# Kernel tuning notes

Hardware: AMD Instinct MI355X
Metric: run time of the kernel (lower is better)

Reference implementation:

```python
import jax, jax.numpy as jnp
import numpy as np

N, E, K, F_IN, H = 50000, 640000, 3, 128, 128


def setup_inputs() -> dict:
    key = jax.random.key(0)
    ks = jax.random.split(key, 14)
    s = 0.05
    return {
        "x": jax.random.normal(ks[0], (N, F_IN), jnp.float32),
        "edge_index": jax.random.randint(ks[1], (2, E), 0, N, dtype=jnp.int32),
        "edge_weight": jax.random.uniform(ks[2], (E,), jnp.float32, minval=0.1, maxval=1.0),
        "W_x": jax.random.normal(ks[3], (4, F_IN, H), jnp.float32) * s,   # dense input weights (i,f,c,o)
        "w_c": jax.random.normal(ks[4], (3, H), jnp.float32) * s,         # peephole weights (i,f,o)
        "b": jax.random.normal(ks[5], (4, H), jnp.float32) * s,           # gate biases (i,f,c,o)
        "theta": jax.random.normal(ks[6], (4, K, H, H), jnp.float32) * s, # ChebConv weights per gate
        "theta_b": jax.random.normal(ks[7], (4, H), jnp.float32) * s,     # ChebConv biases per gate
        "gcn_w": jax.random.normal(ks[8], (H, H), jnp.float32) * s,
        "gcn_b": jnp.zeros((H,), jnp.float32),
        "bn_gamma": jnp.ones((H,), jnp.float32),
        "bn_beta": jnp.zeros((H,), jnp.float32),
        "bn_mean": jax.random.normal(ks[9], (H,), jnp.float32) * 0.1,
        "bn_var": jax.random.uniform(ks[10], (H,), jnp.float32, minval=0.5, maxval=1.5),
        "lin_w": jax.random.normal(ks[11], (H, 1), jnp.float32) * s,
        "lin_b": jnp.zeros((1,), jnp.float32),
    }


def reference(x, edge_index, edge_weight, W_x, w_c, b, theta, theta_b, gcn_w, gcn_b, bn_gamma, bn_beta, bn_mean, bn_var, lin_w, lin_b):
    n = x.shape[0]
    src, dst = edge_index[0], edge_index[1]

    # --- ChebConv normalization (sym, lambda_max=2): L_hat = -D^{-1/2} A D^{-1/2}, zero diagonal ---
    deg = jnp.zeros((n,), x.dtype).at[src].add(edge_weight)
    safe = jnp.where(deg > 0, deg, 1.0)
    dis = jnp.where(deg > 0, jax.lax.rsqrt(safe), 0.0)
    lw = -dis[src] * edge_weight * dis[dst]  # per-edge scaled-Laplacian weight

    def prop(h):  # out[i] = sum_{edges j->i} lw * h[j]
        return jnp.zeros_like(h).at[dst].add(lw[:, None] * h[src])

    def cheb(h, th, tb):  # sum_k T_k(L_hat) h @ theta_k + bias, Chebyshev recurrence
        Tx0, out = h, h @ th[0]
        Tx1 = prop(h)
        out = out + Tx1 @ th[1]
        for k in range(2, K):
            Tx2 = 2.0 * prop(Tx1) - Tx0
            out = out + Tx2 @ th[k]
            Tx0, Tx1 = Tx1, Tx2
        return out + tb

    # --- GCLSTM with H = C = 0 (module passes no initial state) ---
    Hs = jnp.zeros((n, W_x.shape[2]), x.dtype)
    Cs = jnp.zeros_like(Hs)
    I = jax.nn.sigmoid(x @ W_x[0] + cheb(Hs, theta[0], theta_b[0]) + w_c[0] * Cs + b[0])
    Fg = jax.nn.sigmoid(x @ W_x[1] + cheb(Hs, theta[1], theta_b[1]) + w_c[1] * Cs + b[1])
    T = jnp.tanh(x @ W_x[2] + cheb(Hs, theta[2], theta_b[2]) + b[2])
    Cs = Fg * Cs + I * T
    O = jax.nn.sigmoid(x @ W_x[3] + cheb(Hs, theta[3], theta_b[3]) + w_c[2] * Cs + b[3])
    Hs = O * jnp.tanh(Cs)

    # --- GCNConv(H) with unit edge weights + added self-loops ---
    h = Hs @ gcn_w
    deg_g = jnp.ones((n,), x.dtype).at[dst].add(jnp.ones((edge_index.shape[1],), x.dtype))
    dg = jax.lax.rsqrt(deg_g)
    g = jnp.zeros_like(h).at[dst].add((dg[src] * dg[dst])[:, None] * h[src]) + (dg * dg)[:, None] * h + gcn_b

    g = jax.nn.relu(g)
    g = bn_gamma * (g - bn_mean) * jax.lax.rsqrt(bn_var + 1e-5) + bn_beta  # BatchNorm1d (eval)
    return g @ lin_w + lin_b  # Dropout = identity in eval
```

## Files before the change

kernel.cpp:

```cpp
#include <hip/hip_runtime.h>
#include <hip/hip_bf16.h>

#define NN 50000
#define NE 640000
#define CAP 64
#define NGB 782
#define NBIN 782
#define NA 196
#define EPA 3328
#define ORow 784

typedef unsigned short ushort_t;
typedef unsigned int uint_t;
typedef __attribute__((ext_vector_type(8))) short bf16x8;
typedef __attribute__((ext_vector_type(4))) float f32x4;

__device__ __forceinline__ float b2f(ushort_t u) {
    union { uint_t u; float f; } v; v.u = ((uint_t)u) << 16; return v.f;
}
__device__ __forceinline__ ushort_t f2b(float f) {
    union { float f; uint_t u; } v; v.f = f;
    uint_t u = v.u;
    uint_t r = u + 0x7fffu + ((u >> 16) & 1u);
    return (ushort_t)(r >> 16);
}
__device__ __forceinline__ float fsig(float x)  { return __builtin_amdgcn_rcpf(1.0f + __expf(-x)); }
__device__ __forceinline__ float ftanh(float x) { return 1.0f - 2.0f * __builtin_amdgcn_rcpf(1.0f + __expf(2.0f * x)); }
__device__ __forceinline__ float ldm(const void* p, int i, int mf) {
    return mf ? ((const float*)p)[i] : b2f(((const ushort_t*)p)[i]);
}

#define OFF_HB    0
#define OFF_BSRC  12800000
#define OFF_CNT   25600000
#define OFF_CHUNK 25800000
#define OFF_OFFS  28409152
#define OFF_WT    29023808
#define OFF_COEF  29154880
#define OFF_MODE  29157444
#define WS_REQ    29157448

__global__ void fb_k(ushort_t* __restrict__ out, int n) {
    int i = blockIdx.x * blockDim.x + threadIdx.x;
    if (i < n) out[i] = 0;
}

__global__ void prep_k(const ushort_t* __restrict__ x,
                       const void* __restrict__ Wx, const void* __restrict__ gcnw,
                       const void* __restrict__ wc, const void* __restrict__ bb,
                       const void* __restrict__ thb,
                       const void* __restrict__ gam, const void* __restrict__ bet,
                       const void* __restrict__ mea, const void* __restrict__ var,
                       const void* __restrict__ linw, const void* __restrict__ linb,
                       ushort_t* __restrict__ WT, float* __restrict__ coef,
                       int* __restrict__ mode) {
    __shared__ int si[256];
    __shared__ float red[128];
    int b = blockIdx.x, t = threadIdx.x;
    int bad = 0;
    for (int i = t; i < 4096; i += 256) {
        int e = (x[i] >> 7) & 0xFF;
        if (e >= 0xC0) bad++;
    }
    si[t] = bad; __syncthreads();
    for (int o = 128; o >= 1; o >>= 1) { if (t < o) si[t] += si[t + o]; __syncthreads(); }
    int mf = (si[0] > 8) ? 1 : 0;

    if (b < 32) {
        int gid = b * 256 + t;
        int m  = gid >> 11;
        int u  = gid & 2047;
        int k  = u >> 4;
        int f0 = (u & 15) << 3;
        const int srcoff[4] = { 0, 2 * 16384, 3 * 16384, 0 };
        const void* S = (m == 3) ? gcnw : Wx;
        int sbase = srcoff[m] + k * 128 + f0;
        ushort_t vals[8];
        if (mf == 0) {
            bf16x8 v = *(const bf16x8*)((const ushort_t*)S + sbase);
            #pragma unroll
            for (int i = 0; i < 8; i++) vals[i] = (ushort_t)v[i];
        } else {
            const float* Sf = (const float*)S + sbase;
            #pragma unroll
            for (int i = 0; i < 8; i++) vals[i] = f2b(Sf[i]);
        }
        ushort_t* D = WT + m * 16384 + k;
        #pragma unroll
        for (int i = 0; i < 8; i++) D[(f0 + i) * 128] = vals[i];
    } else {
        if (t < 128) {
            float rs = rsqrtf(ldm(var, t, mf) + 1e-5f);
            float ga = ldm(gam, t, mf);
            float lw = ldm(linw, t, mf);
            coef[t]       = ldm(thb, t, mf)           + ldm(bb, t, mf);
            coef[128 + t] = ldm(thb, 2 * 128 + t, mf) + ldm(bb, 2 * 128 + t, mf);
            coef[256 + t] = ldm(thb, 3 * 128 + t, mf) + ldm(bb, 3 * 128 + t, mf);
            coef[384 + t] = ldm(wc, 2 * 128 + t, mf);
            coef[512 + t] = ga * rs * lw;
            red[t] = (ldm(bet, t, mf) - ldm(mea, t, mf) * ga * rs) * lw;
        }
        __syncthreads();
        for (int off = 64; off >= 1; off >>= 1) {
            if (t < off && t < 128) red[t] += red[t + off];
            __syncthreads();
        }
        if (t == 0) {
            coef[640] = red[0] + ldm(linb, 0, mf);
            mode[0] = mf;
        }
    }
}

__launch_bounds__(256)
__global__ void gafi_k(const void* __restrict__ x, const ushort_t* __restrict__ WT,
                       const float* __restrict__ coef, const int* __restrict__ mode,
                       ushort_t* __restrict__ hb,
                       const int* __restrict__ ei, uint_t* __restrict__ chunk,
                       int* __restrict__ offs) {
    __shared__ int sh[4352];
    ushort_t* tile = (ushort_t*)sh;
    int per = blockIdx.x / 5, rem = blockIdx.x % 5;
    int t = threadIdx.x;

    if (rem == 4) {
        int a = per;
        int e0 = a * EPA; if (e0 > NE) e0 = NE;
        int e1 = e0 + EPA; if (e1 > NE) e1 = NE;
        const int* dstp = ei + NE;
        for (int i = t; i < NBIN; i += 256) sh[i] = 0;
        __syncthreads();
        for (int i = e0 + t; i < e1; i += 256) atomicAdd(&sh[dstp[i] >> 6], 1);
        __syncthreads();
        int b0 = t * 4;
        int s = 0;
        #pragma unroll
        for (int j = 0; j < 4; j++) { int bi = b0 + j; if (bi < NBIN) s += sh[bi]; }
        sh[1024 + t] = s;
        __syncthreads();
        for (int off = 1; off < 256; off <<= 1) {
            int v = (t >= off) ? sh[1024 + t - off] : 0;
            __syncthreads();
            sh[1024 + t] += v;
            __syncthreads();
        }
        int run = (t == 0) ? 0 : sh[1024 + t - 1];
        int* orow = offs + a * ORow;
        #pragma unroll
        for (int j = 0; j < 4; j++) {
            int bi = b0 + j;
            if (bi < NBIN) {
                int c = sh[bi];
                orow[bi] = run;
                sh[bi] = run;
                run += c;
            }
        }
        if (t == 0) orow[NBIN] = e1 - e0;
        __syncthreads();
        uint_t* ck = chunk + a * EPA;
        for (int i = e0 + t; i < e1; i += 256) {
            int d = dstp[i], sn = ei[i];
            int pos = atomicAdd(&sh[d >> 6], 1);
            ck[pos] = ((uint_t)sn << 6) | (uint_t)(d & 63);
        }
        return;
    }

    int gb = per * 4 + rem;
    if (gb >= NGB) return;
    int base = gb * 64;
    int mf = mode[0];

    for (int i = 0; i < 4; i++) {
        int idx = (i * 256 + t) * 8;
        int row = idx >> 7, col = idx & 127;
        int n = base + row;
        bf16x8 v;
        if (n >= NN) {
            v = (bf16x8)0;
        } else if (mf == 0) {
            v = *(const bf16x8*)((const ushort_t*)x + n * 128 + col);
        } else {
            const float* xf = (const float*)x + n * 128 + col;
            float4 lo = *(const float4*)xf;
            float4 hi = *(const float4*)(xf + 4);
            v[0] = (short)f2b(lo.x); v[1] = (short)f2b(lo.y);
            v[2] = (short)f2b(lo.z); v[3] = (short)f2b(lo.w);
            v[4] = (short)f2b(hi.x); v[5] = (short)f2b(hi.y);
            v[6] = (short)f2b(hi.z); v[7] = (short)f2b(hi.w);
        }
        *(bf16x8*)&tile[row * 136 + col] = v;
    }
    __syncthreads();

    int lane = t & 63, wave = t >> 6;
    int m = lane & 15, quad = lane >> 4;

    bf16x8 a[4][4];
    #pragma unroll
    for (int rt = 0; rt < 4; rt++)
        #pragma unroll
        for (int kt = 0; kt < 4; kt++)
            a[rt][kt] = *(const bf16x8*)&tile[(rt * 16 + m) * 136 + kt * 32 + quad * 8];
    __syncthreads();

    const ushort_t* WTi = WT;
    const ushort_t* WTc = WT + 16384;
    const ushort_t* WTo = WT + 2 * 16384;

    #pragma unroll
    for (int ft = 0; ft < 2; ft++) {
        int f = wave * 32 + ft * 16 + m;
        bf16x8 bi[4], bc[4], bo[4];
        #pragma unroll
        for (int kt = 0; kt < 4; kt++) {
            int off = f * 128 + kt * 32 + quad * 8;
            bi[kt] = *(const bf16x8*)(WTi + off);
            bc[kt] = *(const bf16x8*)(WTc + off);
            bo[kt] = *(const bf16x8*)(WTo + off);
        }
        float bi_f = coef[f], bc_f = coef[128 + f], bo_f = coef[256 + f], w2 = coef[384 + f];
        #pragma unroll
        for (int rt = 0; rt < 4; rt++) {
            f32x4 ai = {0,0,0,0}, ac = {0,0,0,0}, ao = {0,0,0,0};
            #pragma unroll
            for (int kt = 0; kt < 4; kt++) {
                ai = __builtin_amdgcn_mfma_f32_16x16x32_bf16(a[rt][kt], bi[kt], ai, 0, 0, 0);
                ac = __builtin_amdgcn_mfma_f32_16x16x32_bf16(a[rt][kt], bc[kt], ac, 0, 0, 0);
                ao = __builtin_amdgcn_mfma_f32_16x16x32_bf16(a[rt][kt], bo[kt], ao, 0, 0, 0);
            }
            #pragma unroll
            for (int r = 0; r < 4; r++) {
                float I  = fsig(ai[r] + bi_f);
                float T  = ftanh(ac[r] + bc_f);
                float Cs = I * T;
                float O  = fsig(ao[r] + w2 * Cs + bo_f);
                float Hs = O * ftanh(Cs);
                tile[(rt * 16 + quad * 4 + r) * 136 + f] = f2b(Hs);
            }
        }
    }
    __syncthreads();

    const ushort_t* WTg = WT + 3 * 16384;
    bf16x8 ah[4][4];
    #pragma unroll
    for (int rt = 0; rt < 4; rt++)
        #pragma unroll
        for (int kt = 0; kt < 4; kt++)
            ah[rt][kt] = *(const bf16x8*)&tile[(rt * 16 + m) * 136 + kt * 32 + quad * 8];

    #pragma unroll
    for (int ft = 0; ft < 2; ft++) {
        int f = wave * 32 + ft * 16 + m;
        bf16x8 bg[4];
        #pragma unroll
        for (int kt = 0; kt < 4; kt++)
            bg[kt] = *(const bf16x8*)(WTg + f * 128 + kt * 32 + quad * 8);
        #pragma unroll
        for (int rt = 0; rt < 4; rt++) {
            f32x4 acc = {0,0,0,0};
            #pragma unroll
            for (int kt = 0; kt < 4; kt++)
                acc = __builtin_amdgcn_mfma_f32_16x16x32_bf16(ah[rt][kt], bg[kt], acc, 0, 0, 0);
            #pragma unroll
            for (int r = 0; r < 4; r++) {
                int n = base + rt * 16 + quad * 4 + r;
                if (n < NN) hb[n * 128 + f] = f2b(acc[r]);
            }
        }
    }
}

__launch_bounds__(256)
__global__ void scat_k(const uint_t* __restrict__ chunk, const int* __restrict__ offs,
                       int* __restrict__ bsrc, int* __restrict__ cnt) {
    __shared__ int sstart[NA];
    __shared__ int P[256];
    __shared__ int lcnt[64];
    __shared__ uint_t lbuck[64 * CAP];
    int b = blockIdx.x, t = threadIdx.x;
    int node0 = b << 6;
    if (t < 64) lcnt[t] = 0;
    int len = 0;
    if (t < NA) {
        int st = offs[t * ORow + b];
        int en = offs[t * ORow + b + 1];
        sstart[t] = st;
        len = en - st;
    }
    P[t] = len;
    __syncthreads();
    for (int off = 1; off < 256; off <<= 1) {
        int v = (t >= off) ? P[t - off] : 0;
        __syncthreads();
        P[t] += v;
        __syncthreads();
    }
    int T = P[255];
    for (int i = t; i < T; i += 256) {
        int lo = 0, hi = NA - 1;
        while (lo < hi) { int mid = (lo + hi) >> 1; if (P[mid] > i) hi = mid; else lo = mid + 1; }
        int prev = (lo == 0) ? 0 : P[lo - 1];
        uint_t w = chunk[lo * EPA + sstart[lo] + (i - prev)];
        int d6 = (int)(w & 63u);
        int sn = (int)(w >> 6);
        int p = atomicAdd(&lcnt[d6], 1);
        if (p < CAP) lbuck[(d6 << 6) + p] = (uint_t)sn;
    }
    __syncthreads();
    if (t < 64) { int node = node0 + t; if (node < NN) cnt[node] = lcnt[t]; }
    const int4* lb4 = (const int4*)lbuck;
    int4* bs4 = (int4*)bsrc;
    for (int i = t; i < 1024; i += 256) {
        int node = node0 + (i >> 4);
        if (node < NN) bs4[(node0 << 4) + i] = lb4[i];
    }
}

__launch_bounds__(256)
__global__ void gat_out_k(const ushort_t* __restrict__ hb, const int* __restrict__ cnt,
                          const int* __restrict__ bsrc,
                          const void* __restrict__ gcnb, const float* __restrict__ coef,
                          const int* __restrict__ mode, void* __restrict__ out) {
    int wid  = (blockIdx.x * blockDim.x + threadIdx.x) >> 6;
    int lane = threadIdx.x & 63;
    if (wid >= NN) return;
    int half = lane >> 5, sl = lane & 31;
    int c = cnt[wid]; if (c < 0) c = 0;
    int deg = (c < CAP) ? c : CAP;
    const int* brow = bsrc + wid * CAP;

    float a0 = 0.0f, a1 = 0.0f, a2 = 0.0f, a3 = 0.0f;
    int s0 = brow[half];
    int s1 = brow[half + 2];
    for (int j = half; j < deg; j += 4) {
        int sn0 = brow[(j + 4) & (CAP - 1)];
        int sn1 = brow[(j + 6) & (CAP - 1)];
        {
            int cs = cnt[s0]; if (cs < 0) cs = 0;
            uint2 r = *(const uint2*)(hb + s0 * 128 + sl * 4);
            float w = rsqrtf(1.0f + (float)cs);
            a0 += w * b2f((ushort_t)(r.x & 0xffffu));
            a1 += w * b2f((ushort_t)(r.x >> 16));
            a2 += w * b2f((ushort_t)(r.y & 0xffffu));
            a3 += w * b2f((ushort_t)(r.y >> 16));
        }
        if (j + 2 < deg) {
            int cs = cnt[s1]; if (cs < 0) cs = 0;
            uint2 r = *(const uint2*)(hb + s1 * 128 + sl * 4);
            float w = rsqrtf(1.0f + (float)cs);
            a0 += w * b2f((ushort_t)(r.x & 0xffffu));
            a1 += w * b2f((ushort_t)(r.x >> 16));
            a2 += w * b2f((ushort_t)(r.y & 0xffffu));
            a3 += w * b2f((ushort_t)(r.y >> 16));
        }
        s0 = sn0; s1 = sn1;
    }
    float d = rsqrtf(1.0f + (float)c);
    if (half == 0) {
        uint2 r = *(const uint2*)(hb + wid * 128 + sl * 4);
        a0 += d * b2f((ushort_t)(r.x & 0xffffu));
        a1 += d * b2f((ushort_t)(r.x >> 16));
        a2 += d * b2f((ushort_t)(r.y & 0xffffu));
        a3 += d * b2f((ushort_t)(r.y >> 16));
    }
    a0 += __shfl_xor(a0, 32); a1 += __shfl_xor(a1, 32);
    a2 += __shfl_xor(a2, 32); a3 += __shfl_xor(a3, 32);
    int mf = mode[0];
    int fb = sl * 4;
    float g0 = d * a0 + ldm(gcnb, fb,     mf);
    float g1 = d * a1 + ldm(gcnb, fb + 1, mf);
    float g2 = d * a2 + ldm(gcnb, fb + 2, mf);
    float g3 = d * a3 + ldm(gcnb, fb + 3, mf);
    float v = fmaxf(g0, 0.0f) * coef[512 + fb]
            + fmaxf(g1, 0.0f) * coef[512 + fb + 1]
            + fmaxf(g2, 0.0f) * coef[512 + fb + 2]
            + fmaxf(g3, 0.0f) * coef[512 + fb + 3];
    #pragma unroll
    for (int o = 32; o >= 1; o >>= 1) v += __shfl_down(v, o);
    if (lane == 0) {
        float r = 0.5f * v + coef[640];
        if (mf) ((float*)out)[wid] = r;
        else    ((ushort_t*)out)[wid] = f2b(r);
    }
}

extern "C" void kernel_launch(void* const* d_in, const int* in_sizes, int n_in,
                              void* d_out, int out_size, void* d_ws, size_t ws_size,
                              hipStream_t stream) {
    if (ws_size < (size_t)WS_REQ) {
        fb_k<<<(out_size + 255) / 256, 256, 0, stream>>>((ushort_t*)d_out, out_size);
        return;
    }
    const void* x    = d_in[0];
    const int*  ei   = (const int*)d_in[1];
    const void* Wx   = d_in[3];
    const void* wc   = d_in[4];
    const void* bb   = d_in[5];
    const void* thb  = d_in[7];
    const void* gcnw = d_in[8];
    const void* gcnb = d_in[9];
    const void* gam  = d_in[10];
    const void* bet  = d_in[11];
    const void* mea  = d_in[12];
    const void* var  = d_in[13];
    const void* linw = d_in[14];
    const void* linb = d_in[15];

    char* ws = (char*)d_ws;
    ushort_t* hb    = (ushort_t*)(ws + OFF_HB);
    int*      bsrc  = (int*)     (ws + OFF_BSRC);
    int*      cnt   = (int*)     (ws + OFF_CNT);
    uint_t*   chunk = (uint_t*)  (ws + OFF_CHUNK);
    int*      offs  = (int*)     (ws + OFF_OFFS);
    ushort_t* WT    = (ushort_t*)(ws + OFF_WT);
    float*    coef  = (float*)   (ws + OFF_COEF);
    int*      mode  = (int*)     (ws + OFF_MODE);

    prep_k<<<33, 256, 0, stream>>>((const ushort_t*)x, Wx, gcnw, wc, bb, thb,
                                   gam, bet, mea, var, linw, linb, WT, coef, mode);
    gafi_k<<<NA * 5, 256, 0, stream>>>(x, WT, coef, mode, hb, ei, chunk, offs);
    scat_k<<<NBIN, 256, 0, stream>>>(chunk, offs, bsrc, cnt);
    gat_out_k<<<(NN * 64 + 255) / 256, 256, 0, stream>>>(hb, cnt, bsrc, gcnb, coef, mode, d_out);
}
```

Before: 177.6 us.

## Restructure pipeline: fuse binning into prep, compute counts with GEMM, gather from LDS buckets

Edge binning now runs in the prep kernel, so the gate GEMM kernel only interleaves GEMM blocks with per-bin degree counting. The old scatter kernel and the gather/output kernel are merged: each bin block builds its source buckets in shared memory and its four waves gather and reduce 16 nodes each. This removes the global bsrc array and one launch. The trade-offs are that degree counting reads the chunk array twice, and the gather now runs on fewer, longer-lived blocks with less parallelism per node.

```diff
diff --git a/kernel.cpp b/kernel.cpp
--- a/kernel.cpp
+++ b/kernel.cpp
@@ -31,43 +31,90 @@
 }
 
 #define OFF_HB    0
-#define OFF_BSRC  12800000
-#define OFF_CNT   25600000
-#define OFF_CHUNK 25800000
-#define OFF_OFFS  28409152
-#define OFF_WT    29023808
-#define OFF_COEF  29154880
-#define OFF_MODE  29157444
-#define WS_REQ    29157448
+#define OFF_CHUNK 12800000
+#define OFF_OFFS  15409152
+#define OFF_CNT   16023808
+#define OFF_WT    16223808
+#define OFF_COEF  16354880
+#define OFF_MODE  16357444
+#define WS_REQ    16357448
 
 __global__ void fb_k(ushort_t* __restrict__ out, int n) {
     int i = blockIdx.x * blockDim.x + threadIdx.x;
     if (i < n) out[i] = 0;
 }
 
-__global__ void prep_k(const ushort_t* __restrict__ x,
-                       const void* __restrict__ Wx, const void* __restrict__ gcnw,
-                       const void* __restrict__ wc, const void* __restrict__ bb,
-                       const void* __restrict__ thb,
-                       const void* __restrict__ gam, const void* __restrict__ bet,
-                       const void* __restrict__ mea, const void* __restrict__ var,
-                       const void* __restrict__ linw, const void* __restrict__ linb,
-                       ushort_t* __restrict__ WT, float* __restrict__ coef,
-                       int* __restrict__ mode) {
-    __shared__ int si[256];
+__launch_bounds__(256)
+__global__ void bsprep_k(const ushort_t* __restrict__ x, const int* __restrict__ ei,
+                         const void* __restrict__ Wx, const void* __restrict__ gcnw,
+                         const void* __restrict__ wc, const void* __restrict__ bb,
+                         const void* __restrict__ thb,
+                         const void* __restrict__ gam, const void* __restrict__ bet,
+                         const void* __restrict__ mea, const void* __restrict__ var,
+                         const void* __restrict__ linw, const void* __restrict__ linb,
+                         ushort_t* __restrict__ WT, float* __restrict__ coef,
+                         int* __restrict__ mode,
+                         uint_t* __restrict__ chunk, int* __restrict__ offs) {
+    __shared__ int sh[1280];
     __shared__ float red[128];
     int b = blockIdx.x, t = threadIdx.x;
+
+    if (b < NA) {
+        int a = b;
+        int e0 = a * EPA; if (e0 > NE) e0 = NE;
+        int e1 = e0 + EPA; if (e1 > NE) e1 = NE;
+        const int* dstp = ei + NE;
+        for (int i = t; i < NBIN; i += 256) sh[i] = 0;
+        __syncthreads();
+        for (int i = e0 + t; i < e1; i += 256) atomicAdd(&sh[dstp[i] >> 6], 1);
+        __syncthreads();
+        int b0 = t * 4;
+        int s = 0;
+        #pragma unroll
+        for (int j = 0; j < 4; j++) { int bi = b0 + j; if (bi < NBIN) s += sh[bi]; }
+        sh[1024 + t] = s;
+        __syncthreads();
+        for (int off = 1; off < 256; off <<= 1) {
+            int v = (t >= off) ? sh[1024 + t - off] : 0;
+            __syncthreads();
+            sh[1024 + t] += v;
+            __syncthreads();
+        }
+        int run = (t == 0) ? 0 : sh[1024 + t - 1];
+        int* orow = offs + a * ORow;
+        #pragma unroll
+        for (int j = 0; j < 4; j++) {
+            int bi = b0 + j;
+            if (bi < NBIN) {
+                int c = sh[bi];
+                orow[bi] = run;
+                sh[bi] = run;
+                run += c;
+            }
+        }
+        if (t == 0) orow[NBIN] = e1 - e0;
+        __syncthreads();
+        uint_t* ck = chunk + a * EPA;
+        for (int i = e0 + t; i < e1; i += 256) {
+            int d = dstp[i], sn = ei[i];
+            int pos = atomicAdd(&sh[d >> 6], 1);
+            ck[pos] = ((uint_t)sn << 6) | (uint_t)(d & 63);
+        }
+        return;
+    }
+
     int bad = 0;
     for (int i = t; i < 4096; i += 256) {
         int e = (x[i] >> 7) & 0xFF;
         if (e >= 0xC0) bad++;
     }
-    si[t] = bad; __syncthreads();
-    for (int o = 128; o >= 1; o >>= 1) { if (t < o) si[t] += si[t + o]; __syncthreads(); }
-    int mf = (si[0] > 8) ? 1 : 0;
-
-    if (b < 32) {
-        int gid = b * 256 + t;
+    sh[t] = bad; __syncthreads();
+    for (int o = 128; o >= 1; o >>= 1) { if (t < o) sh[t] += sh[t + o]; __syncthreads(); }
+    int mf = (sh[0] > 8) ? 1 : 0;
+
+    int wb = b - NA;
+    if (wb < 32) {
+        int gid = wb * 256 + t;
         int m  = gid >> 11;
         int u  = gid & 2047;
         int k  = u >> 4;
@@ -113,62 +160,50 @@
 }
 
 __launch_bounds__(256)
-__global__ void gafi_k(const void* __restrict__ x, const ushort_t* __restrict__ WT,
-                       const float* __restrict__ coef, const int* __restrict__ mode,
-                       ushort_t* __restrict__ hb,
-                       const int* __restrict__ ei, uint_t* __restrict__ chunk,
-                       int* __restrict__ offs) {
-    __shared__ int sh[4352];
-    ushort_t* tile = (ushort_t*)sh;
-    int per = blockIdx.x / 5, rem = blockIdx.x % 5;
-    int t = threadIdx.x;
-
-    if (rem == 4) {
-        int a = per;
-        int e0 = a * EPA; if (e0 > NE) e0 = NE;
-        int e1 = e0 + EPA; if (e1 > NE) e1 = NE;
-        const int* dstp = ei + NE;
-        for (int i = t; i < NBIN; i += 256) sh[i] = 0;
-        __syncthreads();
-        for (int i = e0 + t; i < e1; i += 256) atomicAdd(&sh[dstp[i] >> 6], 1);
-        __syncthreads();
-        int b0 = t * 4;
-        int s = 0;
-        #pragma unroll
-        for (int j = 0; j < 4; j++) { int bi = b0 + j; if (bi < NBIN) s += sh[bi]; }
-        sh[1024 + t] = s;
+__global__ void gacnt_k(const void* __restrict__ x, const ushort_t* __restrict__ WT,
+                        const float* __restrict__ coef, const int* __restrict__ mode,
+                        ushort_t* __restrict__ hb,
+                        const uint_t* __restrict__ chunk, const int* __restrict__ offs,
+                        int* __restrict__ cnt) {
+    __shared__ __align__(16) char smem[17408];
+    int b = blockIdx.x, t = threadIdx.x;
+
+    if (b & 1) {
+        int bin = b >> 1;
+        int* P      = (int*)smem;
+        int* sstart = (int*)(smem + 1024);
+        int* lcnt   = (int*)(smem + 1808);
+        if (t < 64) lcnt[t] = 0;
+        int len = 0;
+        if (t < NA) {
+            int st = offs[t * ORow + bin];
+            int en = offs[t * ORow + bin + 1];
+            sstart[t] = st;
+            len = en - st;
+        }
+        P[t] = len;
         __syncthreads();
         for (int off = 1; off < 256; off <<= 1) {
-            int v = (t >= off) ? sh[1024 + t - off] : 0;
+            int v = (t >= off) ? P[t - off] : 0;
             __syncthreads();
-            sh[1024 + t] += v;
+            P[t] += v;
             __syncthreads();
         }
-        int run = (t == 0) ? 0 : sh[1024 + t - 1];
-        int* orow = offs + a * ORow;
-        #pragma unroll
-        for (int j = 0; j < 4; j++) {
-            int bi = b0 + j;
-            if (bi < NBIN) {
-                int c = sh[bi];
-                orow[bi] = run;
-                sh[bi] = run;
-                run += c;
-            }
-        }
-        if (t == 0) orow[NBIN] = e1 - e0;
-        __syncthreads();
-        uint_t* ck = chunk + a * EPA;
-        for (int i = e0 + t; i < e1; i += 256) {
-            int d = dstp[i], sn = ei[i];
-            int pos = atomicAdd(&sh[d >> 6], 1);
-            ck[pos] = ((uint_t)sn << 6) | (uint_t)(d & 63);
-        }
+        int T = P[255];
+        for (int i = t; i < T; i += 256) {
+            int lo = 0, hi = NA - 1;
+            while (lo < hi) { int mid = (lo + hi) >> 1; if (P[mid] > i) hi = mid; else lo = mid + 1; }
+            int prev = (lo == 0) ? 0 : P[lo - 1];
+            uint_t w = chunk[lo * EPA + sstart[lo] + (i - prev)];
+            atomicAdd(&lcnt[(int)(w & 63u)], 1);
+        }
+        __syncthreads();
+        if (t < 64) { int node = (bin << 6) + t; if (node < NN) cnt[node] = lcnt[t]; }
         return;
     }
 
-    int gb = per * 4 + rem;
-    if (gb >= NGB) return;
+    ushort_t* tile = (ushort_t*)smem;
+    int gb = b >> 1;
     int base = gb * 64;
     int mf = mode[0];
 
@@ -274,14 +309,18 @@
 }
 
 __launch_bounds__(256)
-__global__ void scat_k(const uint_t* __restrict__ chunk, const int* __restrict__ offs,
-                       int* __restrict__ bsrc, int* __restrict__ cnt) {
-    __shared__ int sstart[NA];
-    __shared__ int P[256];
-    __shared__ int lcnt[64];
-    __shared__ uint_t lbuck[64 * CAP];
+__global__ void sgat_k(const uint_t* __restrict__ chunk, const int* __restrict__ offs,
+                       const ushort_t* __restrict__ hb, const int* __restrict__ cnt,
+                       const void* __restrict__ gcnb, const float* __restrict__ coef,
+                       const int* __restrict__ mode, void* __restrict__ out) {
+    __shared__ __align__(16) char smem[18448];
+    int* P      = (int*)smem;
+    int* sstart = (int*)(smem + 1024);
+    int* lcnt   = (int*)(smem + 1808);
+    uint_t* lbuck = (uint_t*)(smem + 2064);
     int b = blockIdx.x, t = threadIdx.x;
     int node0 = b << 6;
+
     if (t < 64) lcnt[t] = 0;
     int len = 0;
     if (t < NA) {
@@ -310,80 +349,59 @@
         if (p < CAP) lbuck[(d6 << 6) + p] = (uint_t)sn;
     }
     __syncthreads();
-    if (t < 64) { int node = node0 + t; if (node < NN) cnt[node] = lcnt[t]; }
-    const int4* lb4 = (const int4*)lbuck;
-    int4* bs4 = (int4*)bsrc;
-    for (int i = t; i < 1024; i += 256) {
-        int node = node0 + (i >> 4);
-        if (node < NN) bs4[(node0 << 4) + i] = lb4[i];
-    }
-}
-
-__launch_bounds__(256)
-__global__ void gat_out_k(const ushort_t* __restrict__ hb, const int* __restrict__ cnt,
-                          const int* __restrict__ bsrc,
-                          const void* __restrict__ gcnb, const float* __restrict__ coef,
-                          const int* __restrict__ mode, void* __restrict__ out) {
-    int wid  = (blockIdx.x * blockDim.x + threadIdx.x) >> 6;
-    int lane = threadIdx.x & 63;
-    if (wid >= NN) return;
+
+    int mf = mode[0];
+    int wave = t >> 6, lane = t & 63;
     int half = lane >> 5, sl = lane & 31;
-    int c = cnt[wid]; if (c < 0) c = 0;
-    int deg = (c < CAP) ? c : CAP;
-    const int* brow = bsrc + wid * CAP;
-
-    float a0 = 0.0f, a1 = 0.0f, a2 = 0.0f, a3 = 0.0f;
-    int s0 = brow[half];
-    int s1 = brow[half + 2];
-    for (int j = half; j < deg; j += 4) {
-        int sn0 = brow[(j + 4) & (CAP - 1)];
-        int sn1 = brow[(j + 6) & (CAP - 1)];
-        {
-            int cs = cnt[s0]; if (cs < 0) cs = 0;
-            uint2 r = *(const uint2*)(hb + s0 * 128 + sl * 4);
-            float w = rsqrtf(1.0f + (float)cs);
-            a0 += w * b2f((ushort_t)(r.x & 0xffffu));
-            a1 += w * b2f((ushort_t)(r.x >> 16));
-            a2 += w * b2f((ushort_t)(r.y & 0xffffu));
-            a3 += w * b2f((ushort_t)(r.y >> 16));
-        }
-        if (j + 2 < deg) {
-            int cs = cnt[s1]; if (cs < 0) cs = 0;
-            uint2 r = *(const uint2*)(hb + s1 * 128 + sl * 4);
-            float w = rsqrtf(1.0f + (float)cs);
-            a0 += w * b2f((ushort_t)(r.x & 0xffffu));
-            a1 += w * b2f((ushort_t)(r.x >> 16));
-            a2 += w * b2f((ushort_t)(r.y & 0xffffu));
-            a3 += w * b2f((ushort_t)(r.y >> 16));
-        }
-        s0 = sn0; s1 = sn1;
-    }
-    float d = rsqrtf(1.0f + (float)c);
-    if (half == 0) {
-        uint2 r = *(const uint2*)(hb + wid * 128 + sl * 4);
-        a0 += d * b2f((ushort_t)(r.x & 0xffffu));
-        a1 += d * b2f((ushort_t)(r.x >> 16));
-        a2 += d * b2f((ushort_t)(r.y & 0xffffu));
-        a3 += d * b2f((ushort_t)(r.y >> 16));
-    }
-    a0 += __shfl_xor(a0, 32); a1 += __shfl_xor(a1, 32);
-    a2 += __shfl_xor(a2, 32); a3 += __shfl_xor(a3, 32);
-    int mf = mode[0];
-    int fb = sl * 4;
-    float g0 = d * a0 + ldm(gcnb, fb,     mf);
-    float g1 = d * a1 + ldm(gcnb, fb + 1, mf);
-    float g2 = d * a2 + ldm(gcnb, fb + 2, mf);
-    float g3 = d * a3 + ldm(gcnb, fb + 3, mf);
-    float v = fmaxf(g0, 0.0f) * coef[512 + fb]
-            + fmaxf(g1, 0.0f) * coef[512 + fb + 1]
-            + fmaxf(g2, 0.0f) * coef[512 + fb + 2]
-            + fmaxf(g3, 0.0f) * coef[512 + fb + 3];
-    #pragma unroll
-    for (int o = 32; o >= 1; o >>= 1) v += __shfl_down(v, o);
-    if (lane == 0) {
-        float r = 0.5f * v + coef[640];
-        if (mf) ((float*)out)[wid] = r;
-        else    ((ushort_t*)out)[wid] = f2b(r);
+    for (int q = 0; q < 16; q++) {
+        int local = wave * 16 + q;
+        int wid = node0 + local;
+        if (wid >= NN) break;
+        int c = lcnt[local];
+        int deg = (c < CAP) ? c : CAP;
+        const uint_t* lb = lbuck + (local << 6);
+        float a0 = 0.0f, a1 = 0.0f, a2 = 0.0f, a3 = 0.0f;
+        for (int j = half; j < deg; j += 4) {
+            int ok2 = (j + 2 < deg);
+            int s0 = (int)lb[j];
+            int s1 = (int)lb[ok2 ? j + 2 : j];
+            int cs0 = cnt[s0];
+            int cs1 = cnt[s1];
+            uint2 r0 = *(const uint2*)(hb + s0 * 128 + sl * 4);
+            uint2 r1 = *(const uint2*)(hb + s1 * 128 + sl * 4);
+            float w0 = rsqrtf(1.0f + (float)cs0);
+            float w1 = ok2 ? rsqrtf(1.0f + (float)cs1) : 0.0f;
+            a0 += w0 * b2f((ushort_t)(r0.x & 0xffffu)) + w1 * b2f((ushort_t)(r1.x & 0xffffu));
+            a1 += w0 * b2f((ushort_t)(r0.x >> 16))     + w1 * b2f((ushort_t)(r1.x >> 16));
+            a2 += w0 * b2f((ushort_t)(r0.y & 0xffffu)) + w1 * b2f((ushort_t)(r1.y & 0xffffu));
+            a3 += w0 * b2f((ushort_t)(r0.y >> 16))     + w1 * b2f((ushort_t)(r1.y >> 16));
+        }
+        float d = rsqrtf(1.0f + (float)c);
+        if (half == 0) {
+            uint2 r = *(const uint2*)(hb + wid * 128 + sl * 4);
+            a0 += d * b2f((ushort_t)(r.x & 0xffffu));
+            a1 += d * b2f((ushort_t)(r.x >> 16));
+            a2 += d * b2f((ushort_t)(r.y & 0xffffu));
+            a3 += d * b2f((ushort_t)(r.y >> 16));
+        }
+        a0 += __shfl_xor(a0, 32); a1 += __shfl_xor(a1, 32);
+        a2 += __shfl_xor(a2, 32); a3 += __shfl_xor(a3, 32);
+        int fb = sl * 4;
+        float g0 = d * a0 + ldm(gcnb, fb,     mf);
+        float g1 = d * a1 + ldm(gcnb, fb + 1, mf);
+        float g2 = d * a2 + ldm(gcnb, fb + 2, mf);
+        float g3 = d * a3 + ldm(gcnb, fb + 3, mf);
+        float v = fmaxf(g0, 0.0f) * coef[512 + fb]
+                + fmaxf(g1, 0.0f) * coef[512 + fb + 1]
+                + fmaxf(g2, 0.0f) * coef[512 + fb + 2]
+                + fmaxf(g3, 0.0f) * coef[512 + fb + 3];
+        #pragma unroll
+        for (int o = 32; o >= 1; o >>= 1) v += __shfl_down(v, o);
+        if (lane == 0) {
+            float r = 0.5f * v + coef[640];
+            if (mf) ((float*)out)[wid] = r;
+            else    ((ushort_t*)out)[wid] = f2b(r);
+        }
     }
 }
 
@@ -394,7 +412,7 @@
         fb_k<<<(out_size + 255) / 256, 256, 0, stream>>>((ushort_t*)d_out, out_size);
         return;
     }
-    const void* x    = d_in[0];
+    const ushort_t* x = (const ushort_t*)d_in[0];
     const int*  ei   = (const int*)d_in[1];
     const void* Wx   = d_in[3];
     const void* wc   = d_in[4];
@@ -411,17 +429,16 @@
 
     char* ws = (char*)d_ws;
     ushort_t* hb    = (ushort_t*)(ws + OFF_HB);
-    int*      bsrc  = (int*)     (ws + OFF_BSRC);
-    int*      cnt   = (int*)     (ws + OFF_CNT);
     uint_t*   chunk = (uint_t*)  (ws + OFF_CHUNK);
     int*      offs  = (int*)     (ws + OFF_OFFS);
+    int*      cnt   = (int*)     (ws + OFF_CNT);
     ushort_t* WT    = (ushort_t*)(ws + OFF_WT);
     float*    coef  = (float*)   (ws + OFF_COEF);
     int*      mode  = (int*)     (ws + OFF_MODE);
 
-    prep_k<<<33, 256, 0, stream>>>((const ushort_t*)x, Wx, gcnw, wc, bb, thb,
-                                   gam, bet, mea, var, linw, linb, WT, coef, mode);
-    gafi_k<<<NA * 5, 256, 0, stream>>>(x, WT, coef, mode, hb, ei, chunk, offs);
-    scat_k<<<NBIN, 256, 0, stream>>>(chunk, offs, bsrc, cnt);
-    gat_out_k<<<(NN * 64 + 255) / 256, 256, 0, stream>>>(hb, cnt, bsrc, gcnb, coef, mode, d_out);
-}
+    bsprep_k<<<NA + 33, 256, 0, stream>>>(x, ei, Wx, gcnw, wc, bb, thb,
+                                          gam, bet, mea, var, linw, linb,
+                                          WT, coef, mode, chunk, offs);
+    gacnt_k<<<2 * NGB, 256, 0, stream>>>(x, WT, coef, mode, hb, chunk, offs, cnt);
+    sgat_k<<<NBIN, 256, 0, stream>>>(chunk, offs, hb, cnt, gcnb, coef, mode, d_out);
+}
```

Measured after the change: 203.1 us. +14.3%, slower.

## Restructure GCN gather to full-wave per edge with shuffled neighbor indices

Applied to the files above, without the earlier changes.

The output gather kernel now has each wavefront process one neighbor row at a time across all 64 lanes (2 features per lane), instead of splitting lanes into two halves with 4 features each. Neighbor indices and their normalization weights are loaded once per lane and broadcast by shuffle, unrolled by 8. This removes the cross-half reduction and the serial per-edge loads of index and count. The scatter kernel now zero-fills the local bucket so padded slots are valid, and the workspace layout is reordered. The 0.5 scaling on the final value was dropped, which may reflect a change in how coef is computed or be a bug.

```diff
diff --git a/kernel.cpp b/kernel.cpp
--- a/kernel.cpp
+++ b/kernel.cpp
@@ -32,9 +32,9 @@
 
 #define OFF_HB    0
 #define OFF_BSRC  12800000
-#define OFF_CNT   25600000
-#define OFF_CHUNK 25800000
-#define OFF_OFFS  28409152
+#define OFF_CHUNK 25600000
+#define OFF_OFFS  28209152
+#define OFF_CNT   28823808
 #define OFF_WT    29023808
 #define OFF_COEF  29154880
 #define OFF_MODE  29157444
@@ -283,6 +283,7 @@
     int b = blockIdx.x, t = threadIdx.x;
     int node0 = b << 6;
     if (t < 64) lcnt[t] = 0;
+    for (int i = t; i < 64 * CAP; i += 256) lbuck[i] = 0;
     int len = 0;
     if (t < NA) {
         int st = offs[t * ORow + b];
@@ -327,61 +328,41 @@
     int wid  = (blockIdx.x * blockDim.x + threadIdx.x) >> 6;
     int lane = threadIdx.x & 63;
     if (wid >= NN) return;
-    int half = lane >> 5, sl = lane & 31;
     int c = cnt[wid]; if (c < 0) c = 0;
     int deg = (c < CAP) ? c : CAP;
     const int* brow = bsrc + wid * CAP;
 
-    float a0 = 0.0f, a1 = 0.0f, a2 = 0.0f, a3 = 0.0f;
-    int s0 = brow[half];
-    int s1 = brow[half + 2];
-    for (int j = half; j < deg; j += 4) {
-        int sn0 = brow[(j + 4) & (CAP - 1)];
-        int sn1 = brow[(j + 6) & (CAP - 1)];
-        {
-            int cs = cnt[s0]; if (cs < 0) cs = 0;
-            uint2 r = *(const uint2*)(hb + s0 * 128 + sl * 4);
-            float w = rsqrtf(1.0f + (float)cs);
-            a0 += w * b2f((ushort_t)(r.x & 0xffffu));
-            a1 += w * b2f((ushort_t)(r.x >> 16));
-            a2 += w * b2f((ushort_t)(r.y & 0xffffu));
-            a3 += w * b2f((ushort_t)(r.y >> 16));
-        }
-        if (j + 2 < deg) {
-            int cs = cnt[s1]; if (cs < 0) cs = 0;
-            uint2 r = *(const uint2*)(hb + s1 * 128 + sl * 4);
-            float w = rsqrtf(1.0f + (float)cs);
-            a0 += w * b2f((ushort_t)(r.x & 0xffffu));
-            a1 += w * b2f((ushort_t)(r.x >> 16));
-            a2 += w * b2f((ushort_t)(r.y & 0xffffu));
-            a3 += w * b2f((ushort_t)(r.y >> 16));
-        }
-        s0 = sn0; s1 = sn1;
+    int bv = brow[lane];
+    float wv = 0.0f;
+    if (lane < deg) wv = rsqrtf(1.0f + (float)cnt[bv]);
+
+    float a0 = 0.0f, a1 = 0.0f;
+    for (int j = 0; j < deg; j += 8) {
+        #pragma unroll
+        for (int k = 0; k < 8; k++) {
+            int   s = __shfl(bv, j + k);
+            float w = __shfl(wv, j + k);
+            uint_t r = *(const uint_t*)(hb + s * 128 + lane * 2);
+            a0 += w * b2f((ushort_t)(r & 0xffffu));
+            a1 += w * b2f((ushort_t)(r >> 16));
+        }
     }
     float d = rsqrtf(1.0f + (float)c);
-    if (half == 0) {
-        uint2 r = *(const uint2*)(hb + wid * 128 + sl * 4);
-        a0 += d * b2f((ushort_t)(r.x & 0xffffu));
-        a1 += d * b2f((ushort_t)(r.x >> 16));
-        a2 += d * b2f((ushort_t)(r.y & 0xffffu));
-        a3 += d * b2f((ushort_t)(r.y >> 16));
-    }
-    a0 += __shfl_xor(a0, 32); a1 += __shfl_xor(a1, 32);
-    a2 += __shfl_xor(a2, 32); a3 += __shfl_xor(a3, 32);
+    {
+        uint_t r = *(const uint_t*)(hb + wid * 128 + lane * 2);
+        a0 += d * b2f((ushort_t)(r & 0xffffu));
+        a1 += d * b2f((ushort_t)(r >> 16));
+    }
     int mf = mode[0];
-    int fb = sl * 4;
+    int fb = lane * 2;
     float g0 = d * a0 + ldm(gcnb, fb,     mf);
     float g1 = d * a1 + ldm(gcnb, fb + 1, mf);
-    float g2 = d * a2 + ldm(gcnb, fb + 2, mf);
-    float g3 = d * a3 + ldm(gcnb, fb + 3, mf);
     float v = fmaxf(g0, 0.0f) * coef[512 + fb]
-            + fmaxf(g1, 0.0f) * coef[512 + fb + 1]
-            + fmaxf(g2, 0.0f) * coef[512 + fb + 2]
-            + fmaxf(g3, 0.0f) * coef[512 + fb + 3];
+            + fmaxf(g1, 0.0f) * coef[512 + fb + 1];
     #pragma unroll
     for (int o = 32; o >= 1; o >>= 1) v += __shfl_down(v, o);
     if (lane == 0) {
-        float r = 0.5f * v + coef[640];
+        float r = v + coef[640];
         if (mf) ((float*)out)[wid] = r;
         else    ((ushort_t*)out)[wid] = f2b(r);
     }
@@ -394,7 +375,7 @@
         fb_k<<<(out_size + 255) / 256, 256, 0, stream>>>((ushort_t*)d_out, out_size);
         return;
     }
-    const void* x    = d_in[0];
+    const ushort_t* x = (const ushort_t*)d_in[0];
     const int*  ei   = (const int*)d_in[1];
     const void* Wx   = d_in[3];
     const void* wc   = d_in[4];
@@ -412,14 +393,14 @@
     char* ws = (char*)d_ws;
     ushort_t* hb    = (ushort_t*)(ws + OFF_HB);
     int*      bsrc  = (int*)     (ws + OFF_BSRC);
-    int*      cnt   = (int*)     (ws + OFF_CNT);
     uint_t*   chunk = (uint_t*)  (ws + OFF_CHUNK);
     int*      offs  = (int*)     (ws + OFF_OFFS);
+    int*      cnt   = (int*)     (ws + OFF_CNT);
     ushort_t* WT    = (ushort_t*)(ws + OFF_WT);
     float*    coef  = (float*)   (ws + OFF_COEF);
     int*      mode  = (int*)     (ws + OFF_MODE);
 
-    prep_k<<<33, 256, 0, stream>>>((const ushort_t*)x, Wx, gcnw, wc, bb, thb,
+    prep_k<<<33, 256, 0, stream>>>(x, Wx, gcnw, wc, bb, thb,
                                    gam, bet, mea, var, linw, linb, WT, coef, mode);
     gafi_k<<<NA * 5, 256, 0, stream>>>(x, WT, coef, mode, hb, ei, chunk, offs);
     scat_k<<<NBIN, 256, 0, stream>>>(chunk, offs, bsrc, cnt);
```

New measurement: 165.0 us, median of 3. 7.1% less time.
